# Performance work log

Measured on AMD Instinct MI355X. Metric: run time of the kernel, lower is better.

Reference implementation:

```python
import jax, jax.numpy as jnp
import numpy as np

HIDDEN = 1024
N_HEAD = 16
D_HEAD = HIDDEN // N_HEAD


def setup_inputs() -> dict:
    key = jax.random.key(0)
    k1, k2, k3, k4, k5, k6, k7 = jax.random.split(key, 7)
    B, Sq, Sk = 8, 1024, 1024
    decoder_input = jax.random.normal(k1, (B, Sq, HIDDEN), dtype=jnp.float32)
    encoder_output = jax.random.normal(k2, (B, Sk, HIDDEN), dtype=jnp.float32)
    # torch.rand -> uniform [0,1) for the per-head projection params
    W_query = jax.random.uniform(k3, (N_HEAD, D_HEAD, HIDDEN), dtype=jnp.float32)
    W_key = jax.random.uniform(k4, (N_HEAD, D_HEAD, HIDDEN), dtype=jnp.float32)
    W_value = jax.random.uniform(k5, (N_HEAD, D_HEAD, HIDDEN), dtype=jnp.float32)
    # nn.Linear default init: U(-1/sqrt(fan_in), 1/sqrt(fan_in))
    bound = 1.0 / np.sqrt(HIDDEN)
    W_out = jax.random.uniform(k6, (HIDDEN, HIDDEN), dtype=jnp.float32, minval=-bound, maxval=bound)
    b_out = jax.random.uniform(k7, (HIDDEN,), dtype=jnp.float32, minval=-bound, maxval=bound)
    return {
        "decoder_input": decoder_input,
        "encoder_output": encoder_output,
        "W_query": W_query,
        "W_key": W_key,
        "W_value": W_value,
        "W_out": W_out,
        "b_out": b_out,
    }


def reference(decoder_input, encoder_output, W_query, W_key, W_value, W_out, b_out):
    # per-head projections, vectorized over heads: x @ W[i].T == einsum over hidden
    q = jnp.einsum("bqh,ndh->bnqd", decoder_input, W_query)   # [B,N,Sq,D]
    k = jnp.einsum("bkh,ndh->bnkd", encoder_output, W_key)    # [B,N,Sk,D]
    v = jnp.einsum("bkh,ndh->bnkd", encoder_output, W_value)  # [B,N,Sk,D]
    scores = jnp.einsum("bnqd,bnkd->bnqk", q, k) / jnp.sqrt(jnp.float32(D_HEAD))
    attn = jax.nn.softmax(scores, axis=-1)                     # [B,N,Sq,Sk]
    heads = jnp.einsum("bnqk,bnkd->bnqd", attn, v)             # [B,N,Sq,D]
    B, N, Sq, D = heads.shape
    concat = jnp.transpose(heads, (0, 2, 1, 3)).reshape(B, Sq, N * D)  # [B,Sq,H]
    out = concat @ W_out.T + b_out
    return out
```

## Files before the change

### kernel.cpp

```cpp
#include <hip/hip_runtime.h>
#include <hip/hip_bf16.h>
#include <math.h>

#define HID 1024
#define NH 16
#define DH 64
#define BATCH 8
#define SEQ 1024
#define MTOT (BATCH * SEQ)

typedef __attribute__((ext_vector_type(8))) short bfrag;
typedef __attribute__((ext_vector_type(4))) float f32x4;
typedef __attribute__((ext_vector_type(8))) unsigned short us8;
typedef __attribute__((ext_vector_type(4))) unsigned short us4;
typedef __attribute__((ext_vector_type(2))) unsigned int u32x2;
typedef unsigned int u32;
typedef unsigned short u16;

#define SCALE_Q 0.18033688011112042f

__device__ __forceinline__ u16 f2b(float f) {
    u32 u = __float_as_uint(f);
    return (u16)((u + 0x7FFFu + ((u >> 16) & 1u)) >> 16);
}
__device__ __forceinline__ float b2f(u16 h) { return __uint_as_float(((u32)h) << 16); }

__device__ __forceinline__ u32 packbf(float a, float b) {
    __hip_bfloat162 t = __float22bfloat162_rn(float2{a, b});
    u32 r;
    __builtin_memcpy(&r, &t, 4);
    return r;
}

__device__ __forceinline__ void gl_lds16(const void* g, void* l) {
    __builtin_amdgcn_global_load_lds(
        (const __attribute__((address_space(1))) unsigned int*)g,
        (__attribute__((address_space(3))) unsigned int*)l, 16, 0, 0);
}

__device__ __forceinline__ u32 swz(u32 L) { return L ^ (((L >> 6) & 7u) << 4); }
__device__ __forceinline__ u32 unswz(u32 p) {
    u32 b = ((((p >> 6) ^ (p >> 8)) & 1u) << 4) | (((p >> 7) & 1u) << 5) | (((p >> 8) & 1u) << 6);
    return p ^ b;
}
__device__ __forceinline__ u32 swz128(u32 L) { return L ^ (((L >> 7) & 7u) << 4); }

__global__ __launch_bounds__(256) void prep(
    const float* __restrict__ enc,
    const float* __restrict__ Wq, const float* __restrict__ Wk,
    const float* __restrict__ Wv, const float* __restrict__ Wo,
    u16* __restrict__ Eh,
    u16* __restrict__ Wqh, u16* __restrict__ Wql,
    u16* __restrict__ Wkh, u16* __restrict__ Wkl,
    u16* __restrict__ Wvh, u16* __restrict__ Woh)
{
    const int NX4 = MTOT * HID / 4;
    const int NW4 = HID * HID / 4;
    const int total = NX4 + 4 * NW4;
    for (int i = blockIdx.x * blockDim.x + threadIdx.x; i < total;
         i += gridDim.x * blockDim.x) {
        if (i < NX4) {
            float4 f = ((const float4*)enc)[i];
            us4 h;
            h[0] = f2b(f.x); h[1] = f2b(f.y); h[2] = f2b(f.z); h[3] = f2b(f.w);
            ((us4*)Eh)[i] = h;
        } else {
            int j = i - NX4;
            int rgn = j / NW4, k = j - rgn * NW4;
            const float* src = (rgn == 0) ? Wq : (rgn == 1) ? Wk : (rgn == 2) ? Wv : Wo;
            float4 f = ((const float4*)src)[k];
            float v[4] = {f.x, f.y, f.z, f.w};
            us4 h, l;
#pragma unroll
            for (int q = 0; q < 4; ++q) {
                u16 hh = f2b(v[q]);
                h[q] = hh;
                l[q] = f2b(v[q] - b2f(hh));
            }
            if (rgn == 0) { ((us4*)Wqh)[k] = h; ((us4*)Wql)[k] = l; }
            else if (rgn == 1) { ((us4*)Wkh)[k] = h; ((us4*)Wkl)[k] = l; }
            else if (rgn == 2) { ((us4*)Wvh)[k] = h; }
            else { ((us4*)Woh)[k] = h; }
        }
    }
}

template <int TERMS, int XMODE, int EPI>
__global__ __launch_bounds__(256) void gemm_mfma(
    const float* __restrict__ Xf, const u16* __restrict__ Xb,
    const u16* __restrict__ Wh, const u16* __restrict__ Wl,
    const float* __restrict__ bias, float scale,
    float* __restrict__ Of, u16* __restrict__ O1, u16* __restrict__ O2)
{
    constexpr u32 OFF_AH = 0, OFF_BH = 8192, OFF_AL = 16384, OFF_BL = 24576;
    __shared__ __align__(16) char smem[(TERMS == 3) ? 32768 : 16384];

    u32 bid = blockIdx.x;
    u32 wg = (bid & 7) * 64 + (bid >> 3);
    const u32 m0 = (wg >> 3) * 128, n0 = (wg & 7) * 128;

    const int tid = threadIdx.x;
    const int w = tid >> 6, lane = tid & 63, c = lane & 15, g = lane >> 4;
    const int wr = w >> 1, wc = w & 1;

    u32 pa[4], pb[4];
#pragma unroll
    for (int i = 0; i < 4; ++i) {
        pa[i] = swz((u32)(wr * 64 + i * 16 + c) * 64 + (u32)g * 16);
        pb[i] = swz((u32)(wc * 64 + i * 16 + c) * 64 + (u32)g * 16);
    }

    f32x4 acc[4][4];
#pragma unroll
    for (int i = 0; i < 4; ++i)
#pragma unroll
        for (int j = 0; j < 4; ++j) acc[i][j] = f32x4{0.f, 0.f, 0.f, 0.f};

    for (int kb = 0; kb < HID / 32; ++kb) {
        const int koff = kb * 32;
        {
            const int nB = (TERMS == 3) ? 16 : 8;
            const int total = nB + ((XMODE == 1) ? 8 : 0);
            for (int id = w; id < total; id += 4) {
                u32 p = (u32)(id & 7) * 1024 + (u32)lane * 16;
                u32 L = unswz(p);
                u32 row = L >> 6, colb = L & 63;
                const char* src;
                u32 loff;
                if (id < 8) {
                    src = (const char*)Wh + ((size_t)(n0 + row)) * 2048 + (size_t)koff * 2 + colb;
                    loff = OFF_BH + (p & 0xFFFFFC00u);
                } else if (TERMS == 3 && id < 16) {
                    src = (const char*)Wl + ((size_t)(n0 + row)) * 2048 + (size_t)koff * 2 + colb;
                    loff = OFF_BL + (p & 0xFFFFFC00u);
                } else {
                    src = (const char*)Xb + ((size_t)(m0 + row)) * 2048 + (size_t)koff * 2 + colb;
                    loff = OFF_AH + (p & 0xFFFFFC00u);
                }
                gl_lds16(src, smem + loff);
            }
        }
        if (XMODE == 0) {
            const int row = tid >> 1, half = tid & 1;
            const float* xr = Xf + ((size_t)(m0 + row)) * HID + koff + half * 16;
            float4 f0 = ((const float4*)xr)[0], f1 = ((const float4*)xr)[1],
                   f2 = ((const float4*)xr)[2], f3 = ((const float4*)xr)[3];
            float v[16] = {f0.x, f0.y, f0.z, f0.w, f1.x, f1.y, f1.z, f1.w,
                           f2.x, f2.y, f2.z, f2.w, f3.x, f3.y, f3.z, f3.w};
#pragma unroll
            for (int s = 0; s < 2; ++s) {
                us8 h, l8;
#pragma unroll
                for (int i = 0; i < 8; ++i) {
                    u16 hh = f2b(v[s * 8 + i]);
                    h[i] = hh;
                    if (TERMS == 3) l8[i] = f2b(v[s * 8 + i] - b2f(hh));
                }
                u32 ph = swz((u32)row * 64 + (u32)half * 32 + (u32)s * 16);
                *(us8*)(smem + OFF_AH + ph) = h;
                if (TERMS == 3) *(us8*)(smem + OFF_AL + ph) = l8;
            }
        }
        __syncthreads();
        bfrag ah[4], al[4];
#pragma unroll
        for (int mi = 0; mi < 4; ++mi) {
            ah[mi] = *(const bfrag*)(smem + OFF_AH + pa[mi]);
            if (TERMS == 3) al[mi] = *(const bfrag*)(smem + OFF_AL + pa[mi]);
        }
#pragma unroll
        for (int ni = 0; ni < 4; ++ni) {
            bfrag bh = *(const bfrag*)(smem + OFF_BH + pb[ni]);
            bfrag bl;
            if (TERMS == 3) bl = *(const bfrag*)(smem + OFF_BL + pb[ni]);
#pragma unroll
            for (int mi = 0; mi < 4; ++mi) {
                acc[mi][ni] = __builtin_amdgcn_mfma_f32_16x16x32_bf16(ah[mi], bh, acc[mi][ni], 0, 0, 0);
                if (TERMS == 3) {
                    acc[mi][ni] = __builtin_amdgcn_mfma_f32_16x16x32_bf16(ah[mi], bl, acc[mi][ni], 0, 0, 0);
                    acc[mi][ni] = __builtin_amdgcn_mfma_f32_16x16x32_bf16(al[mi], bh, acc[mi][ni], 0, 0, 0);
                }
            }
        }
        __syncthreads();
    }
#pragma unroll
    for (int mi = 0; mi < 4; ++mi) {
#pragma unroll
        for (int ni = 0; ni < 4; ++ni) {
            const u32 n = n0 + wc * 64 + ni * 16 + c;
            const u32 mb = m0 + wr * 64 + mi * 16 + 4 * g;
            if (EPI == 0) {
                float bv = bias[n];
#pragma unroll
                for (int r = 0; r < 4; ++r)
                    Of[(size_t)(mb + r) * HID + n] = acc[mi][ni][r] + bv;
            } else if (EPI == 2) {
                const u32 h = n >> 6, d = n & 63;
                const u32 b_ = mb >> 10, s = mb & 1023;
                size_t base = ((size_t)(b_ * NH + h) * SEQ + s) * 64 + d;
#pragma unroll
                for (int r = 0; r < 4; ++r) {
                    float v = acc[mi][ni][r] * scale;
                    u16 hh = f2b(v);
                    O1[base + (size_t)r * 64] = hh;
                    O2[base + (size_t)r * 64] = f2b(v - b2f(hh));
                }
            } else {
                const u32 h = n >> 6, d = n & 63;
                const u32 b_ = mb >> 10, s = mb & 1023;
                us4 o;
#pragma unroll
                for (int r = 0; r < 4; ++r) o[r] = f2b(acc[mi][ni][r]);
                *(us4*)&O1[((size_t)(b_ * NH + h) * 64 + d) * SEQ + s] = o;
            }
        }
    }
}

__global__ __launch_bounds__(256) void attn_mfma(
    const u16* __restrict__ Qh, const u16* __restrict__ Ql,
    const u16* __restrict__ Kh, const u16* __restrict__ Kl,
    const u16* __restrict__ Vt, u16* __restrict__ Cc)
{
    __shared__ __align__(16) u16 sQH[4096], sQL[4096], sKH[4096], sKL[4096], sVT[4096];
    __shared__ __align__(16) char sPw[8192];

    u32 bid = blockIdx.x;
    u32 wg = (bid & 7) * 256 + (bid >> 3);
    const int b = wg >> 8;
    const int head = (wg >> 4) & 15;
    const int q0 = (wg & 15) * 64;

    const int tid = threadIdx.x;
    const int w = tid >> 6, lane = tid & 63, c = lane & 15, g = lane >> 4;

    const size_t hb = (size_t)(b * NH + head);
    const char* gQH = (const char*)(Qh + (hb * SEQ + q0) * 64);
    const char* gQL = (const char*)(Ql + (hb * SEQ + q0) * 64);
    const char* gKH = (const char*)(Kh + hb * SEQ * 64);
    const char* gKL = (const char*)(Kl + hb * SEQ * 64);
    const char* gVT = (const char*)(Vt + hb * 64 * SEQ);

    for (int t = w; t < 16; t += 4) {
        u32 seg = (u32)(t & 7);
        u32 ps = swz128(seg * 1024 + (u32)lane * 16);
        const char* src = ((t < 8) ? gQH : gQL) + ps;
        u16* dst = ((t < 8) ? sQH : sQL) + seg * 512;
        gl_lds16(src, dst);
    }

    const u32 ps0 = swz128((u32)w * 1024 + (u32)lane * 16);
    const u32 ps1 = swz128((u32)(w + 4) * 1024 + (u32)lane * 16);
    const char* pKH0 = gKH + ps0;  const char* pKH1 = gKH + ps1;
    const char* pKL0 = gKL + ps0;  const char* pKL1 = gKL + ps1;
    const char* pVT0 = gVT + (size_t)(ps0 >> 7) * (SEQ * 2) + (ps0 & 127);
    const char* pVT1 = gVT + (size_t)(ps1 >> 7) * (SEQ * 2) + (ps1 & 127);
    u16* dKH0 = sKH + w * 512;        u16* dKH1 = sKH + (w + 4) * 512;
    u16* dKL0 = sKL + w * 512;        u16* dKL1 = sKL + (w + 4) * 512;
    u16* dVT0 = sVT + w * 512;        u16* dVT1 = sVT + (w + 4) * 512;

    char* pwBase = sPw + w * 2048;
    const u32 pwRow = (u32)c * 128;
    const u32 pwX = ((u32)(c & 7)) << 4;

    float m_ = -1e30f, l_ = 0.f;
    f32x4 acc[4];
#pragma unroll
    for (int j = 0; j < 4; ++j) acc[j] = f32x4{0.f, 0.f, 0.f, 0.f};
    bfrag qh[2], ql[2];

    for (int kc = 0; kc < SEQ / 64; ++kc) {
        __syncthreads();
        gl_lds16(pKH0, dKH0); gl_lds16(pKH1, dKH1);
        gl_lds16(pKL0, dKL0); gl_lds16(pKL1, dKL1);
        gl_lds16(pVT0, dVT0); gl_lds16(pVT1, dVT1);
        pKH0 += 8192; pKH1 += 8192; pKL0 += 8192; pKL1 += 8192;
        pVT0 += 128;  pVT1 += 128;
        __syncthreads();

        if (kc == 0) {
#pragma unroll
            for (int ks = 0; ks < 2; ++ks) {
                u32 aoff = swz128((u32)(w * 16 + c) * 128 + (u32)ks * 64 + (u32)g * 16);
                qh[ks] = *(const bfrag*)((const char*)sQH + aoff);
                ql[ks] = *(const bfrag*)((const char*)sQL + aoff);
            }
        }

        f32x4 s4[4];
#pragma unroll
        for (int j = 0; j < 4; ++j) s4[j] = f32x4{0.f, 0.f, 0.f, 0.f};
#pragma unroll
        for (int ks = 0; ks < 2; ++ks) {
#pragma unroll
            for (int jf = 0; jf < 4; ++jf) {
                u32 koff = swz128((u32)(jf * 16 + c) * 128 + (u32)ks * 64 + (u32)g * 16);
                bfrag kh_ = *(const bfrag*)((const char*)sKH + koff);
                bfrag kl_ = *(const bfrag*)((const char*)sKL + koff);
                s4[jf] = __builtin_amdgcn_mfma_f32_16x16x32_bf16(kh_, qh[ks], s4[jf], 0, 0, 0);
                s4[jf] = __builtin_amdgcn_mfma_f32_16x16x32_bf16(kl_, qh[ks], s4[jf], 0, 0, 0);
                s4[jf] = __builtin_amdgcn_mfma_f32_16x16x32_bf16(kh_, ql[ks], s4[jf], 0, 0, 0);
            }
        }

        float pmax = s4[0][0];
#pragma unroll
        for (int jf = 0; jf < 4; ++jf)
#pragma unroll
            for (int r = 0; r < 4; ++r) pmax = fmaxf(pmax, s4[jf][r]);
        pmax = fmaxf(pmax, __shfl_xor(pmax, 16));
        pmax = fmaxf(pmax, __shfl_xor(pmax, 32));

        if (!__all(pmax <= m_ + 8.f)) {
            float mn = fmaxf(m_, pmax);
            float scl = exp2f(m_ - mn);
            m_ = mn;
            l_ *= scl;
#pragma unroll
            for (int jd = 0; jd < 4; ++jd) {
                f32x4 t = acc[jd];
                t[0] *= scl; t[1] *= scl; t[2] *= scl; t[3] *= scl;
                acc[jd] = t;
            }
        }

        float p[16];
        float rs = 0.f;
#pragma unroll
        for (int jf = 0; jf < 4; ++jf)
#pragma unroll
            for (int r = 0; r < 4; ++r) {
                float pv = exp2f(s4[jf][r] - m_);
                p[jf * 4 + r] = pv;
                rs += pv;
            }
        rs += __shfl_xor(rs, 16);
        rs += __shfl_xor(rs, 32);
        l_ += rs;

#pragma unroll
        for (int jf = 0; jf < 4; ++jf) {
            u32 w0 = packbf(p[jf * 4 + 0], p[jf * 4 + 1]);
            u32 w1 = packbf(p[jf * 4 + 2], p[jf * 4 + 3]);
            u32 off = (pwRow + (u32)(32 * jf + 8 * g)) ^ pwX;
            *(u32x2*)(pwBase + off) = u32x2{w0, w1};
        }

#pragma unroll
        for (int ks = 0; ks < 2; ++ks) {
            u32 roff = (pwRow + (u32)(64 * ks + 16 * g)) ^ pwX;
            bfrag pf = *(const bfrag*)(pwBase + roff);
#pragma unroll
            for (int jd = 0; jd < 4; ++jd) {
                u32 voff = swz128((u32)(jd * 16 + c) * 128 + (u32)ks * 64 + (u32)g * 16);
                bfrag vv = *(const bfrag*)((const char*)sVT + voff);
                acc[jd] = __builtin_amdgcn_mfma_f32_16x16x32_bf16(vv, pf, acc[jd], 0, 0, 0);
            }
        }
    }

    float inv = 1.f / l_;
    size_t rowb = ((size_t)(b * SEQ + q0 + w * 16 + c)) * HID + head * DH;
#pragma unroll
    for (int jd = 0; jd < 4; ++jd) {
        us4 o;
#pragma unroll
        for (int r = 0; r < 4; ++r) o[r] = f2b(acc[jd][r] * inv);
        *(us4*)&Cc[rowb + jd * 16 + 4 * g] = o;
    }
}

extern "C" void kernel_launch(void* const* d_in, const int* in_sizes, int n_in,
                              void* d_out, int out_size, void* d_ws, size_t ws_size,
                              hipStream_t stream)
{
    const float* dec = (const float*)d_in[0];
    const float* enc = (const float*)d_in[1];
    const float* Wq = (const float*)d_in[2];
    const float* Wk = (const float*)d_in[3];
    const float* Wv = (const float*)d_in[4];
    const float* Wo = (const float*)d_in[5];
    const float* bo = (const float*)d_in[6];
    float* out = (float*)d_out;

    char* ws = (char*)d_ws;
    const size_t MB = 1u << 20;
    u16* Eh  = (u16*)ws;
    u16* Qhg = (u16*)(ws + 16 * MB);
    u16* Qlg = (u16*)(ws + 32 * MB);
    u16* Khg = (u16*)(ws + 48 * MB);
    u16* Klg = (u16*)(ws + 64 * MB);
    u16* Vtg = (u16*)(ws + 80 * MB);
    u16* Wqh = (u16*)(ws + 96 * MB);
    u16* Wql = Wqh + (1u << 20);
    u16* Wkh = Wql + (1u << 20);
    u16* Wkl = Wkh + (1u << 20);
    u16* Wvh = Wkl + (1u << 20);
    u16* Woh = Wvh + (1u << 20);
    u16* Cc  = Eh;

    prep<<<2048, 256, 0, stream>>>(enc, Wq, Wk, Wv, Wo,
                                   Eh, Wqh, Wql, Wkh, Wkl, Wvh, Woh);

    gemm_mfma<3, 0, 2><<<512, 256, 0, stream>>>(dec, nullptr, Wqh, Wql, nullptr,
                                                SCALE_Q, nullptr, Qhg, Qlg);
    gemm_mfma<3, 0, 2><<<512, 256, 0, stream>>>(enc, nullptr, Wkh, Wkl, nullptr,
                                                1.0f, nullptr, Khg, Klg);
    gemm_mfma<1, 1, 3><<<512, 256, 0, stream>>>(nullptr, Eh, Wvh, nullptr, nullptr,
                                                1.0f, nullptr, Vtg, nullptr);

    attn_mfma<<<2048, 256, 0, stream>>>(Qhg, Qlg, Khg, Klg, Vtg, Cc);

    gemm_mfma<1, 1, 0><<<512, 256, 0, stream>>>(nullptr, Cc, Woh, nullptr, bo,
                                                1.0f, out, nullptr, nullptr);
}
```

Baseline: 417.4 us.

## Double-buffer K/V tiles in attention and use hardware exp2 with MFMA priority

The attention kernel now keeps two LDS buffers for the K-high, K-low and V tiles. The next 64-key chunk is loaded with global_load_lds while the current chunk is being computed, which halves the barriers per chunk and overlaps load latency with MFMA and softmax work. Q is first staged through one of the buffers, and the swizzled K/V offsets are computed once before the loop. exp2f is replaced by a raw v_exp_f32, and s_setprio raises wave priority around the MFMA blocks. The cost is more LDS per block, which may lower occupancy, and the hardware exp skips the library's range handling.

```diff
diff --git a/kernel.cpp b/kernel.cpp
--- a/kernel.cpp
+++ b/kernel.cpp
@@ -29,6 +29,12 @@
     __hip_bfloat162 t = __float22bfloat162_rn(float2{a, b});
     u32 r;
     __builtin_memcpy(&r, &t, 4);
+    return r;
+}
+
+__device__ __forceinline__ float exp2_hw(float x) {
+    float r;
+    asm("v_exp_f32 %0, %1" : "=v"(r) : "v"(x));
     return r;
 }
 
@@ -223,7 +229,7 @@
     const u16* __restrict__ Kh, const u16* __restrict__ Kl,
     const u16* __restrict__ Vt, u16* __restrict__ Cc)
 {
-    __shared__ __align__(16) u16 sQH[4096], sQL[4096], sKH[4096], sKL[4096], sVT[4096];
+    __shared__ __align__(16) char sBuf[2][24576];
     __shared__ __align__(16) char sPw[8192];
 
     u32 bid = blockIdx.x;
@@ -242,13 +248,8 @@
     const char* gKL = (const char*)(Kl + hb * SEQ * 64);
     const char* gVT = (const char*)(Vt + hb * 64 * SEQ);
 
-    for (int t = w; t < 16; t += 4) {
-        u32 seg = (u32)(t & 7);
-        u32 ps = swz128(seg * 1024 + (u32)lane * 16);
-        const char* src = ((t < 8) ? gQH : gQL) + ps;
-        u16* dst = ((t < 8) ? sQH : sQL) + seg * 512;
-        gl_lds16(src, dst);
-    }
+    char* b0 = sBuf[0];
+    char* b1 = sBuf[1];
 
     const u32 ps0 = swz128((u32)w * 1024 + (u32)lane * 16);
     const u32 ps1 = swz128((u32)(w + 4) * 1024 + (u32)lane * 16);
@@ -256,9 +257,40 @@
     const char* pKL0 = gKL + ps0;  const char* pKL1 = gKL + ps1;
     const char* pVT0 = gVT + (size_t)(ps0 >> 7) * (SEQ * 2) + (ps0 & 127);
     const char* pVT1 = gVT + (size_t)(ps1 >> 7) * (SEQ * 2) + (ps1 & 127);
-    u16* dKH0 = sKH + w * 512;        u16* dKH1 = sKH + (w + 4) * 512;
-    u16* dKL0 = sKL + w * 512;        u16* dKL1 = sKL + (w + 4) * 512;
-    u16* dVT0 = sVT + w * 512;        u16* dVT1 = sVT + (w + 4) * 512;
+    const u32 d0 = (u32)w * 1024, d1 = (u32)(w + 4) * 1024;
+
+    auto STAGE = [&](char* bb) {
+        gl_lds16(pKH0, bb + d0);          gl_lds16(pKH1, bb + d1);
+        gl_lds16(pKL0, bb + 8192 + d0);   gl_lds16(pKL1, bb + 8192 + d1);
+        gl_lds16(pVT0, bb + 16384 + d0);  gl_lds16(pVT1, bb + 16384 + d1);
+        pKH0 += 8192; pKH1 += 8192; pKL0 += 8192; pKL1 += 8192;
+        pVT0 += 128;  pVT1 += 128;
+    };
+
+    for (int t = w; t < 16; t += 4) {
+        u32 seg = (u32)(t & 7);
+        u32 ps = swz128(seg * 1024 + (u32)lane * 16);
+        const char* src = ((t < 8) ? gQH : gQL) + ps;
+        gl_lds16(src, b1 + ((t < 8) ? 0u : 8192u) + seg * 1024);
+    }
+    STAGE(b0);
+    __syncthreads();
+
+    bfrag qh[2], ql[2];
+#pragma unroll
+    for (int ks = 0; ks < 2; ++ks) {
+        u32 aoff = swz128((u32)(w * 16 + c) * 128 + (u32)ks * 64 + (u32)g * 16);
+        qh[ks] = *(const bfrag*)(b1 + aoff);
+        ql[ks] = *(const bfrag*)(b1 + 8192 + aoff);
+    }
+    __syncthreads();
+
+    u32 koff[2][4];
+#pragma unroll
+    for (int ks = 0; ks < 2; ++ks)
+#pragma unroll
+        for (int jf = 0; jf < 4; ++jf)
+            koff[ks][jf] = swz128((u32)(jf * 16 + c) * 128 + (u32)ks * 64 + (u32)g * 16);
 
     char* pwBase = sPw + w * 2048;
     const u32 pwRow = (u32)c * 128;
@@ -268,41 +300,24 @@
     f32x4 acc[4];
 #pragma unroll
     for (int j = 0; j < 4; ++j) acc[j] = f32x4{0.f, 0.f, 0.f, 0.f};
-    bfrag qh[2], ql[2];
-
-    for (int kc = 0; kc < SEQ / 64; ++kc) {
-        __syncthreads();
-        gl_lds16(pKH0, dKH0); gl_lds16(pKH1, dKH1);
-        gl_lds16(pKL0, dKL0); gl_lds16(pKL1, dKL1);
-        gl_lds16(pVT0, dVT0); gl_lds16(pVT1, dVT1);
-        pKH0 += 8192; pKH1 += 8192; pKL0 += 8192; pKL1 += 8192;
-        pVT0 += 128;  pVT1 += 128;
-        __syncthreads();
-
-        if (kc == 0) {
-#pragma unroll
-            for (int ks = 0; ks < 2; ++ks) {
-                u32 aoff = swz128((u32)(w * 16 + c) * 128 + (u32)ks * 64 + (u32)g * 16);
-                qh[ks] = *(const bfrag*)((const char*)sQH + aoff);
-                ql[ks] = *(const bfrag*)((const char*)sQL + aoff);
-            }
-        }
-
+
+    auto COMPUTE = [&](const char* bb) {
         f32x4 s4[4];
 #pragma unroll
         for (int j = 0; j < 4; ++j) s4[j] = f32x4{0.f, 0.f, 0.f, 0.f};
+        __builtin_amdgcn_s_setprio(1);
 #pragma unroll
         for (int ks = 0; ks < 2; ++ks) {
 #pragma unroll
             for (int jf = 0; jf < 4; ++jf) {
-                u32 koff = swz128((u32)(jf * 16 + c) * 128 + (u32)ks * 64 + (u32)g * 16);
-                bfrag kh_ = *(const bfrag*)((const char*)sKH + koff);
-                bfrag kl_ = *(const bfrag*)((const char*)sKL + koff);
+                bfrag kh_ = *(const bfrag*)(bb + koff[ks][jf]);
+                bfrag kl_ = *(const bfrag*)(bb + 8192 + koff[ks][jf]);
                 s4[jf] = __builtin_amdgcn_mfma_f32_16x16x32_bf16(kh_, qh[ks], s4[jf], 0, 0, 0);
                 s4[jf] = __builtin_amdgcn_mfma_f32_16x16x32_bf16(kl_, qh[ks], s4[jf], 0, 0, 0);
                 s4[jf] = __builtin_amdgcn_mfma_f32_16x16x32_bf16(kh_, ql[ks], s4[jf], 0, 0, 0);
             }
         }
+        __builtin_amdgcn_s_setprio(0);
 
         float pmax = s4[0][0];
 #pragma unroll
@@ -314,7 +329,7 @@
 
         if (!__all(pmax <= m_ + 8.f)) {
             float mn = fmaxf(m_, pmax);
-            float scl = exp2f(m_ - mn);
+            float scl = exp2_hw(m_ - mn);
             m_ = mn;
             l_ *= scl;
 #pragma unroll
@@ -331,7 +346,7 @@
         for (int jf = 0; jf < 4; ++jf)
 #pragma unroll
             for (int r = 0; r < 4; ++r) {
-                float pv = exp2f(s4[jf][r] - m_);
+                float pv = exp2_hw(s4[jf][r] - m_);
                 p[jf * 4 + r] = pv;
                 rs += pv;
             }
@@ -351,13 +366,23 @@
         for (int ks = 0; ks < 2; ++ks) {
             u32 roff = (pwRow + (u32)(64 * ks + 16 * g)) ^ pwX;
             bfrag pf = *(const bfrag*)(pwBase + roff);
+            __builtin_amdgcn_s_setprio(1);
 #pragma unroll
             for (int jd = 0; jd < 4; ++jd) {
-                u32 voff = swz128((u32)(jd * 16 + c) * 128 + (u32)ks * 64 + (u32)g * 16);
-                bfrag vv = *(const bfrag*)((const char*)sVT + voff);
+                bfrag vv = *(const bfrag*)(bb + 16384 + koff[ks][jd]);
                 acc[jd] = __builtin_amdgcn_mfma_f32_16x16x32_bf16(vv, pf, acc[jd], 0, 0, 0);
             }
-        }
+            __builtin_amdgcn_s_setprio(0);
+        }
+    };
+
+    for (int it = 0; it < 8; ++it) {
+        STAGE(b1);
+        COMPUTE(b0);
+        __syncthreads();
+        if (it < 7) STAGE(b0);
+        COMPUTE(b1);
+        if (it < 7) __syncthreads();
     }
 
     float inv = 1.f / l_;
```

Measured after the change: 417.1 us. About the same (-0.1%).
